# Optimization experiments

Hardware: AMD Instinct MI355X
Metric: run time of the kernel (lower is better)

## Reference

```python
import jax, jax.numpy as jnp
import numpy as np
from jax import lax

NUM_SIMS = 2048
NUM_BITS = 256   # == num_nodes
MID_DIM = 512
LN_EPS = 1e-5


def _net(x, w1, b1, gamma, beta, w2, b2):
    # BnMLP: Linear -> GELU (exact erf) -> LayerNorm -> Linear -> Sigmoid
    h = x @ w1 + b1                                   # [S, MID]
    h = jax.nn.gelu(h, approximate=False)
    mu = jnp.mean(h, axis=-1, keepdims=True)
    var = jnp.mean(jnp.square(h - mu), axis=-1, keepdims=True)
    h = (h - mu) * lax.rsqrt(var + LN_EPS) * gamma + beta
    return jax.nn.sigmoid(h @ w2 + b2)                # [S, NUM_BITS]


def setup_inputs() -> dict:
    key = jax.random.key(0)
    k_x, k_p, k_w1, k_w2 = jax.random.split(key, 4)
    xs_flt = jax.random.uniform(k_x, (NUM_SIMS, NUM_BITS), dtype=jnp.float32)
    # one random permutation of the nodes per simulation (th.randperm per sim)
    ids_ary = jax.vmap(lambda k: jax.random.permutation(k, NUM_BITS))(
        jax.random.split(k_p, NUM_SIMS)).astype(jnp.int32)   # [S, N]
    w1 = jax.random.normal(k_w1, (NUM_BITS, MID_DIM), jnp.float32) / np.sqrt(NUM_BITS)
    b1 = jnp.full((MID_DIM,), 1e-6, jnp.float32)
    gamma = jnp.ones((MID_DIM,), jnp.float32)
    beta = jnp.zeros((MID_DIM,), jnp.float32)
    w2 = jax.random.normal(k_w2, (MID_DIM, NUM_BITS), jnp.float32) * (0.1 / np.sqrt(MID_DIM))
    b2 = jnp.full((NUM_BITS,), 1e-6, jnp.float32)
    return {"xs_flt": xs_flt, "ids_ary": ids_ary, "w1": w1, "b1": b1,
            "gamma": gamma, "beta": beta, "w2": w2, "b2": b2}


def reference(xs_flt, ids_ary, w1, b1, gamma, beta, w2, b2):
    # gathers prob at (sim, ids[sim]) and writes ps broadcast over all rows at
    # columns ids (faithful to torch's `probs[:, ids] = ps` broadcast semantics).
    def step(probs, ids):
        out = _net(probs, w1, b1, gamma, beta, w2, b2)        # [S, N]
        ps = jnp.take_along_axis(out, ids[:, None], axis=1)[:, 0]  # [S]
        probs = probs.at[:, ids].set(ps)                      # broadcast over rows
        return probs, None

    probs, _ = lax.scan(step, xs_flt, ids_ary.T)              # scan over N nodes
    return probs
```

## Files before the change

### kernel.cpp

```cpp
#include <hip/hip_runtime.h>
#include <math.h>

#define S_ 2048
#define N_ 256
#define MID_ 512
#define NB_ 8
#define JSL_ 64
#define LN_EPS_ 1e-5f
#define NBLK_ 64
#define NSTEP_ 253
#define BSTRIDE_ 288
#define SLOT_F_ (NB_*BSTRIDE_)
#define TAGW_ 32

typedef float f32x4 __attribute__((ext_vector_type(4)));
typedef float f32x2 __attribute__((ext_vector_type(2)));

__device__ __forceinline__ float gelu_exact(float x){
    return 0.5f * x * (1.0f + erff(x * 0.70710678118654752440f));
}

__device__ __forceinline__ int atomic_read_l2(int* p){
    int v; int zero = 0;
    asm volatile("global_atomic_add %0, %1, %2, off sc0\n\ts_waitcnt vmcnt(0)"
                 : "=v"(v) : "v"(p), "v"(zero) : "memory");
    return v;
}


__global__ void k_init(const float* __restrict__ xs, const float* __restrict__ w2,
                       float* __restrict__ probs, float* __restrict__ w2T,
                       unsigned int* __restrict__ wmask32, int* __restrict__ tagsall)
{
    int idx = blockIdx.x * blockDim.x + threadIdx.x;
    if (idx < S_*N_) probs[idx] = xs[idx];
    if (idx < MID_*N_) {
        int j = idx / N_, c = idx % N_;
        w2T[c*MID_ + j] = w2[idx];
    }
    if (idx < (N_*N_)/4) wmask32[idx] = 0u;
    if (idx < NSTEP_*TAGW_ + 8) tagsall[idx] = 0;
    if (idx == 0) tagsall[NSTEP_*TAGW_ + 8] = -1;
}

__global__ void k_mask(const int* __restrict__ ids, unsigned char* __restrict__ wmask){
    int i = blockIdx.x*blockDim.x + threadIdx.x;
    if (i < S_*N_){
        int t = i & (N_-1);
        int c = ids[i];
        wmask[t*N_ + c] = 1;
    }
}

__global__ void k_pack(const unsigned char* __restrict__ wmask,
                       unsigned int* __restrict__ wmaskb){
    int d = blockIdx.x*blockDim.x + threadIdx.x;
    if (d < (N_*N_)/32){
        const unsigned int* p = (const unsigned int*)(wmask + d*32);
        unsigned int bits = 0;
        #pragma unroll
        for (int k = 0; k < 8; k++){
            unsigned int v = p[k];
            if (v & 0x000000FFu) bits |= 1u << (k*4 + 0);
            if (v & 0x0000FF00u) bits |= 1u << (k*4 + 1);
            if (v & 0x00FF0000u) bits |= 1u << (k*4 + 2);
            if (v & 0xFF000000u) bits |= 1u << (k*4 + 3);
        }
        wmaskb[d] = bits;
    }
}

__global__ void k_ab(const float* __restrict__ gamma, const float* __restrict__ beta,
                     const float* __restrict__ w2, const float* __restrict__ b2,
                     float* __restrict__ A, float* __restrict__ Bc){
    __shared__ float ra[256], rb[256];
    int c = blockIdx.x, tid = threadIdx.x;
    float a = 0.f, b = 0.f;
    for (int j = tid; j < MID_; j += 256){
        float v = w2[j*N_ + c];
        a += gamma[j]*v;
        b += beta[j]*v;
    }
    ra[tid] = a; rb[tid] = b; __syncthreads();
    for (int off = 128; off > 0; off >>= 1){
        if (tid < off){ ra[tid] += ra[tid+off]; rb[tid] += rb[tid+off]; }
        __syncthreads();
    }
    if (tid == 0){ A[c] = ra[0]; Bc[c] = rb[0] + b2[c]; }
}


__global__ __launch_bounds__(256) void k_full_rows(
    const float* __restrict__ probs, const float* __restrict__ w1,
    const float* __restrict__ b1, const float* __restrict__ gamma,
    const float* __restrict__ beta, const float* __restrict__ w2T,
    const float* __restrict__ b2, const int* __restrict__ ids,
    float* __restrict__ ps, int t)
{
    __shared__ float prow[8][N_];
    int tid = threadIdx.x;
    int r0 = blockIdx.x * 8;
    for (int i = tid; i < 8*N_; i += 256)
        prow[i>>8][i&255] = probs[(r0 + (i>>8))*N_ + (i&255)];
    __syncthreads();
    int r = tid >> 5, jg = tid & 31;
    float h[16];
    #pragma unroll
    for (int m = 0; m < 16; m++) h[m] = b1[jg + 32*m];
    for (int c = 0; c < N_; c++){
        float p = prow[r][c];
        const float* w1r = w1 + c*MID_;
        #pragma unroll
        for (int m = 0; m < 16; m++) h[m] = fmaf(p, w1r[jg + 32*m], h[m]);
    }
    float s1 = 0.f, s2 = 0.f;
    #pragma unroll
    for (int m = 0; m < 16; m++){
        float g = gelu_exact(h[m]);
        h[m] = g; s1 += g; s2 += g*g;
    }
    #pragma unroll
    for (int off = 16; off > 0; off >>= 1){
        s1 += __shfl_xor(s1, off, 32);
        s2 += __shfl_xor(s2, off, 32);
    }
    float mu  = s1 * (1.f/MID_);
    float var = s2 * (1.f/MID_) - mu*mu;
    float inv = rsqrtf(var + LN_EPS_);
    int rg = r0 + r;
    int id = ids[rg*N_ + t];
    const float* wrow = w2T + id*MID_;
    float acc = 0.f;
    #pragma unroll
    for (int m = 0; m < 16; m++){
        int j = jg + 32*m;
        float hn = (h[m] - mu)*inv*gamma[j] + beta[j];
        acc = fmaf(hn, wrow[j], acc);
    }
    #pragma unroll
    for (int off = 16; off > 0; off >>= 1) acc += __shfl_xor(acc, off, 32);
    if (jg == 0) ps[rg] = 1.f/(1.f + expf(-(acc + b2[id])));
}

__global__ void k_scatter(const int* __restrict__ ids, const float* __restrict__ ps,
                          float* __restrict__ newval, int* __restrict__ wrote, int t){
    __shared__ int lastk[N_];
    int tid = threadIdx.x;
    lastk[tid] = -1;
    __syncthreads();
    for (int k = tid; k < S_; k += 256) atomicMax(&lastk[ids[k*N_ + t]], k);
    __syncthreads();
    int lk = lastk[tid];
    wrote[tid] = (lk >= 0) ? 1 : 0;
    if (lk >= 0) newval[tid] = ps[lk];
}

__global__ void k_apply(float* __restrict__ probs, const float* __restrict__ newval,
                        const int* __restrict__ wrote){
    int idx = blockIdx.x*blockDim.x + threadIdx.x;
    int c = idx & (N_-1);
    if (wrote[c]) probs[idx] = newval[c];
}


__global__ __launch_bounds__(512) void k_fast(
    const float* __restrict__ w1, const float* __restrict__ b1,
    const float* __restrict__ gamma, const float* __restrict__ w2,
    const float* __restrict__ A, const float* __restrict__ Bc,
    const unsigned int* __restrict__ wmaskb, const float* __restrict__ probs,
    float* __restrict__ slots, int* __restrict__ tags,
    int* __restrict__ cnt, int* __restrict__ winner,
    float* __restrict__ commonFinal, int t0)
{
    __shared__ int s_role;
    __shared__ __attribute__((aligned(16))) float commonS[N_];
    __shared__ __attribute__((aligned(16))) float gvals[JSL_];
    __shared__ float ws8[16];
    __shared__ float pst[NB_][2];
    __shared__ unsigned int wbits[(N_*N_)/32];

    int tid = threadIdx.x;

    if (tid == 0){
        int xcd;
        asm volatile("s_getreg_b32 %0, hwreg(HW_REG_XCC_ID)" : "=s"(xcd));
        xcd &= 7;
        int pos = atomicAdd(&cnt[xcd], 1);
        int role = -1;
        if (pos == NB_ - 1){
            int old = atomicCAS(winner, -1, xcd);
            if (old == -1) role = NB_ - 1;
        } else if (pos < NB_ - 1){
            int w;
            while ((w = atomicCAS(winner, -2, -2)) == -1)
                __builtin_amdgcn_s_sleep(2);
            if (w == xcd) role = pos;
        }
        s_role = role;
    }
    __syncthreads();
    int role = s_role;
    if (role < 0) return;
    int j0 = role * JSL_;

    int l = tid & 63, w = tid >> 6;
    int cg = l & 7;
    int jA = (w<<3) + (l>>3);
    int cB = w*32 + (l & 31);
    int khalf = l >> 5;

    float w1r[32];
    #pragma unroll
    for (int cc = 0; cc < 32; cc++)
        w1r[cc] = w1[(cg*32 + cc)*MID_ + j0 + jA];
    float g2r[32];
    #pragma unroll
    for (int kk = 0; kk < 32; kk++)
        g2r[kk] = gamma[j0 + khalf*32 + kk] * w2[(j0 + khalf*32 + kk)*N_ + cB];
    float b1v = b1[j0 + jA];

    for (int i = tid; i < (N_*N_)/32; i += 512) wbits[i] = wmaskb[i];
    if (tid < N_) commonS[tid ^ (((tid>>5)&7)<<2)] = probs[tid];
    float Ac  = (tid < N_) ? A[tid]  : 0.f;
    float Bcc = (tid < N_) ? Bc[tid] : 0.f;
    __syncthreads();

    for (int t = t0; t < N_; t++){
        int si = t - t0;
        float* slot = slots + si*SLOT_F_;
        float* myp  = slot + role*BSTRIDE_;
        {
            float a0=0.f, a1=0.f, a2=0.f, a3=0.f;
            #pragma unroll
            for (int cc = 0; cc < 8; cc++){
                f32x4 cv = *(const f32x4*)(&commonS[(cg*32 + cc*4) ^ (cg<<2)]);
                a0 = fmaf(w1r[cc*4+0], cv.x, a0);
                a1 = fmaf(w1r[cc*4+1], cv.y, a1);
                a2 = fmaf(w1r[cc*4+2], cv.z, a2);
                a3 = fmaf(w1r[cc*4+3], cv.w, a3);
            }
            float hp = (a0+a1) + (a2+a3);
            hp += __shfl_xor(hp, 1);
            hp += __shfl_xor(hp, 2);
            hp += __shfl_xor(hp, 4);
            float g = gelu_exact(hp + b1v);
            float s1 = g, s2 = g*g;
            s1 += __shfl_xor(s1, 8);  s2 += __shfl_xor(s2, 8);
            s1 += __shfl_xor(s1, 16); s2 += __shfl_xor(s2, 16);
            s1 += __shfl_xor(s1, 32); s2 += __shfl_xor(s2, 32);
            if (l == 0){ ws8[w*2] = s1; ws8[w*2+1] = s2; }
            if (cg == 0) gvals[jA] = g;
        }
        __syncthreads();
        {
            float p0=0.f, p1=0.f, p2=0.f, p3=0.f;
            #pragma unroll
            for (int kk = 0; kk < 8; kk++){
                f32x4 gv = *(const f32x4*)(&gvals[khalf*32 + kk*4]);
                p0 = fmaf(g2r[kk*4+0], gv.x, p0);
                p1 = fmaf(g2r[kk*4+1], gv.y, p1);
                p2 = fmaf(g2r[kk*4+2], gv.z, p2);
                p3 = fmaf(g2r[kk*4+3], gv.w, p3);
            }
            float p = (p0+p1) + (p2+p3);
            p += __shfl_xor(p, 32);
            if (l < 32) myp[cB] = p;
        }
        if (tid == 0){
            float S1 = 0.f, S2 = 0.f;
            #pragma unroll
            for (int ww = 0; ww < 8; ww++){ S1 += ws8[ww*2]; S2 += ws8[ww*2+1]; }
            f32x2 st; st.x = S1; st.y = S2;
            *(f32x2*)(myp + 256) = st;
        }
        asm volatile("s_waitcnt vmcnt(0)" ::: "memory");
        __syncthreads();
        if (tid == 0)
            *(volatile int*)(tags + si*TAGW_ + role) = t + 1;
        if (tid < NB_){
            int* tp = tags + si*TAGW_ + tid;
            while (atomic_read_l2(tp) < t + 1) {}
            f32x2 st = *(const f32x2*)(slot + tid*BSTRIDE_ + 256);
            pst[tid][0] = st.x; pst[tid][1] = st.y;
        }
        __syncthreads();
        if (tid < N_){
            const float* sp = slot + tid;
            float s1 = 0.f;
            #pragma unroll
            for (int bb = 0; bb < NB_; bb++) s1 += sp[bb*BSTRIDE_];
            float S1 = 0.f, S2 = 0.f;
            #pragma unroll
            for (int bb = 0; bb < NB_; bb++){ S1 += pst[bb][0]; S2 += pst[bb][1]; }
            float mu  = S1 * (1.f/MID_);
            float var = S2 * (1.f/MID_) - mu*mu;
            float inv = rsqrtf(var + LN_EPS_);
            float s = inv*(s1 - mu*Ac) + Bcc;
            float o = 1.f/(1.f + expf(-s));
            if ((wbits[(t<<3) + (tid>>5)] >> (tid&31)) & 1u)
                commonS[tid ^ (((tid>>5)&7)<<2)] = o;
        }
        __syncthreads();
    }
    if (role == 0 && tid < N_)
        commonFinal[tid] = commonS[tid ^ (((tid>>5)&7)<<2)];
}

__global__ void k_out(const float* __restrict__ commonFinal, float* __restrict__ out){
    int idx = blockIdx.x*blockDim.x + threadIdx.x;
    out[idx] = commonFinal[idx & (N_-1)];
}


extern "C" void kernel_launch(void* const* d_in, const int* in_sizes, int n_in,
                              void* d_out, int out_size, void* d_ws, size_t ws_size,
                              hipStream_t stream)
{
    const float* xs    = (const float*)d_in[0];
    const int*   ids   = (const int*)  d_in[1];
    const float* w1    = (const float*)d_in[2];
    const float* b1    = (const float*)d_in[3];
    const float* gamma = (const float*)d_in[4];
    const float* beta  = (const float*)d_in[5];
    const float* w2    = (const float*)d_in[6];
    const float* b2    = (const float*)d_in[7];
    float* out = (float*)d_out;

    float* ws      = (float*)d_ws;
    float* probs   = ws;
    float* slots   = ws + 2048;
    float* w2T     = ws + 524288;
    float* A       = ws + 786432;
    float* Bc      = ws + 786688;
    float* ps      = ws + 786944;
    float* newval  = ws + 788992;
    int*   wrote   = (int*)(ws + 789248);
    unsigned char* wmask = (unsigned char*)(ws + 789504);
    unsigned int* wmaskb = (unsigned int*)(ws + 805888);
    int*   tagsall = (int*)(ws + 807936);
    int*   tags    = tagsall;
    int*   cnt     = tagsall + NSTEP_*TAGW_;
    int*   winner  = cnt + 8;
    float* commonFinal = ws + 816064;

    k_init<<<2048, 256, 0, stream>>>(xs, w2, probs, w2T,
                                     (unsigned int*)wmask, tagsall);
    k_mask<<<2048, 256, 0, stream>>>(ids, wmask);
    k_ab<<<256, 256, 0, stream>>>(gamma, beta, w2, b2, A, Bc);
    k_pack<<<8, 256, 0, stream>>>(wmask, wmaskb);

    for (int t = 0; t < 3; t++){
        k_full_rows<<<256, 256, 0, stream>>>(probs, w1, b1, gamma, beta, w2T, b2,
                                             ids, ps, t);
        k_scatter<<<1, 256, 0, stream>>>(ids, ps, newval, wrote, t);
        k_apply<<<2048, 256, 0, stream>>>(probs, newval, wrote);
    }

    k_fast<<<NBLK_, 512, 0, stream>>>(w1, b1, gamma, w2, A, Bc, wmaskb, probs,
                                      slots, tags, cnt, winner, commonFinal, 3);
    k_out<<<2048, 256, 0, stream>>>(commonFinal, out);
}
```

Baseline: 702.8 us.

## Use packed 64-bit counter barrier and fold mask and final apply into other kernels

Replaces the per-block tag flags, polled by eight threads with atomic reads, with a single 64-bit counter per step. Each of the eight blocks adds one byte, and thread 0 spins with s_sleep until every byte is set. The byte mask is now built directly with atomicOr, which drops the separate pack kernel. The last k_apply is skipped by having k_fast read newval and wrote when it initialises its state. The barrier now funnels all eight blocks through one atomic address and adds an extra __syncthreads per step, which may change the latency of the per-step handshake.

```diff
diff --git a/kernel.cpp b/kernel.cpp
--- a/kernel.cpp
+++ b/kernel.cpp
@@ -11,7 +11,8 @@
 #define NSTEP_ 253
 #define BSTRIDE_ 288
 #define SLOT_F_ (NB_*BSTRIDE_)
-#define TAGW_ 32
+#define TAGST_ 16
+#define TAG_TARGET_ 0x0101010101010101ULL
 
 typedef float f32x4 __attribute__((ext_vector_type(4)));
 typedef float f32x2 __attribute__((ext_vector_type(2)));
@@ -20,17 +21,11 @@
     return 0.5f * x * (1.0f + erff(x * 0.70710678118654752440f));
 }
 
-__device__ __forceinline__ int atomic_read_l2(int* p){
-    int v; int zero = 0;
-    asm volatile("global_atomic_add %0, %1, %2, off sc0\n\ts_waitcnt vmcnt(0)"
-                 : "=v"(v) : "v"(p), "v"(zero) : "memory");
-    return v;
-}
-
 
 __global__ void k_init(const float* __restrict__ xs, const float* __restrict__ w2,
                        float* __restrict__ probs, float* __restrict__ w2T,
-                       unsigned int* __restrict__ wmask32, int* __restrict__ tagsall)
+                       unsigned int* __restrict__ wmaskb, int* __restrict__ tagw32,
+                       int* __restrict__ cnt, int* __restrict__ winner)
 {
     int idx = blockIdx.x * blockDim.x + threadIdx.x;
     if (idx < S_*N_) probs[idx] = xs[idx];
@@ -38,35 +33,18 @@
         int j = idx / N_, c = idx % N_;
         w2T[c*MID_ + j] = w2[idx];
     }
-    if (idx < (N_*N_)/4) wmask32[idx] = 0u;
-    if (idx < NSTEP_*TAGW_ + 8) tagsall[idx] = 0;
-    if (idx == 0) tagsall[NSTEP_*TAGW_ + 8] = -1;
-}
-
-__global__ void k_mask(const int* __restrict__ ids, unsigned char* __restrict__ wmask){
+    if (idx < (N_*N_)/32) wmaskb[idx] = 0u;
+    if (idx < NSTEP_*TAGST_*2) tagw32[idx] = 0;
+    if (idx < 8) cnt[idx] = 0;
+    if (idx == 0) *winner = -1;
+}
+
+__global__ void k_maskb(const int* __restrict__ ids, unsigned int* __restrict__ wmaskb){
     int i = blockIdx.x*blockDim.x + threadIdx.x;
     if (i < S_*N_){
         int t = i & (N_-1);
         int c = ids[i];
-        wmask[t*N_ + c] = 1;
-    }
-}
-
-__global__ void k_pack(const unsigned char* __restrict__ wmask,
-                       unsigned int* __restrict__ wmaskb){
-    int d = blockIdx.x*blockDim.x + threadIdx.x;
-    if (d < (N_*N_)/32){
-        const unsigned int* p = (const unsigned int*)(wmask + d*32);
-        unsigned int bits = 0;
-        #pragma unroll
-        for (int k = 0; k < 8; k++){
-            unsigned int v = p[k];
-            if (v & 0x000000FFu) bits |= 1u << (k*4 + 0);
-            if (v & 0x0000FF00u) bits |= 1u << (k*4 + 1);
-            if (v & 0x00FF0000u) bits |= 1u << (k*4 + 2);
-            if (v & 0xFF000000u) bits |= 1u << (k*4 + 3);
-        }
-        wmaskb[d] = bits;
+        atomicOr(&wmaskb[(t<<3) + (c>>5)], 1u << (c&31));
     }
 }
 
@@ -168,7 +146,8 @@
     const float* __restrict__ gamma, const float* __restrict__ w2,
     const float* __restrict__ A, const float* __restrict__ Bc,
     const unsigned int* __restrict__ wmaskb, const float* __restrict__ probs,
-    float* __restrict__ slots, int* __restrict__ tags,
+    const float* __restrict__ newval, const int* __restrict__ wrote,
+    float* __restrict__ slots, unsigned long long* __restrict__ tagw,
     int* __restrict__ cnt, int* __restrict__ winner,
     float* __restrict__ commonFinal, int t0)
 {
@@ -220,7 +199,8 @@
     float b1v = b1[j0 + jA];
 
     for (int i = tid; i < (N_*N_)/32; i += 512) wbits[i] = wmaskb[i];
-    if (tid < N_) commonS[tid ^ (((tid>>5)&7)<<2)] = probs[tid];
+    if (tid < N_)
+        commonS[tid ^ (((tid>>5)&7)<<2)] = wrote[tid] ? newval[tid] : probs[tid];
     float Ac  = (tid < N_) ? A[tid]  : 0.f;
     float Bcc = (tid < N_) ? Bc[tid] : 0.f;
     __syncthreads();
@@ -275,11 +255,14 @@
         }
         asm volatile("s_waitcnt vmcnt(0)" ::: "memory");
         __syncthreads();
-        if (tid == 0)
-            *(volatile int*)(tags + si*TAGW_ + role) = t + 1;
+        if (tid == 0){
+            unsigned long long* tp = tagw + si*TAGST_;
+            atomicAdd(tp, 1ULL << (8*role));
+            while (atomicAdd(tp, 0ULL) != TAG_TARGET_)
+                __builtin_amdgcn_s_sleep(1);
+        }
+        __syncthreads();
         if (tid < NB_){
-            int* tp = tags + si*TAGW_ + tid;
-            while (atomic_read_l2(tp) < t + 1) {}
             f32x2 st = *(const f32x2*)(slot + tid*BSTRIDE_ + 256);
             pst[tid][0] = st.x; pst[tid][1] = st.y;
         }
@@ -335,28 +318,27 @@
     float* ps      = ws + 786944;
     float* newval  = ws + 788992;
     int*   wrote   = (int*)(ws + 789248);
-    unsigned char* wmask = (unsigned char*)(ws + 789504);
     unsigned int* wmaskb = (unsigned int*)(ws + 805888);
-    int*   tagsall = (int*)(ws + 807936);
-    int*   tags    = tagsall;
-    int*   cnt     = tagsall + NSTEP_*TAGW_;
+    int*   tagw32  = (int*)(ws + 807936);
+    unsigned long long* tagw = (unsigned long long*)tagw32;
+    int*   cnt     = tagw32 + NSTEP_*TAGST_*2;
     int*   winner  = cnt + 8;
     float* commonFinal = ws + 816064;
 
-    k_init<<<2048, 256, 0, stream>>>(xs, w2, probs, w2T,
-                                     (unsigned int*)wmask, tagsall);
-    k_mask<<<2048, 256, 0, stream>>>(ids, wmask);
+    k_init<<<2048, 256, 0, stream>>>(xs, w2, probs, w2T, wmaskb, tagw32,
+                                     cnt, winner);
+    k_maskb<<<2048, 256, 0, stream>>>(ids, wmaskb);
     k_ab<<<256, 256, 0, stream>>>(gamma, beta, w2, b2, A, Bc);
-    k_pack<<<8, 256, 0, stream>>>(wmask, wmaskb);
 
     for (int t = 0; t < 3; t++){
         k_full_rows<<<256, 256, 0, stream>>>(probs, w1, b1, gamma, beta, w2T, b2,
                                              ids, ps, t);
         k_scatter<<<1, 256, 0, stream>>>(ids, ps, newval, wrote, t);
-        k_apply<<<2048, 256, 0, stream>>>(probs, newval, wrote);
+        if (t < 2) k_apply<<<2048, 256, 0, stream>>>(probs, newval, wrote);
     }
 
     k_fast<<<NBLK_, 512, 0, stream>>>(w1, b1, gamma, w2, A, Bc, wmaskb, probs,
-                                      slots, tags, cnt, winner, commonFinal, 3);
+                                      newval, wrote, slots, tagw, cnt, winner,
+                                      commonFinal, 3);
     k_out<<<2048, 256, 0, stream>>>(commonFinal, out);
 }
```

New measurement: 723.2 us. +2.9%, slower.
